# Kernel tuning notes

Hardware: AMD Instinct MI355X
Metric: run time of the kernel (lower is better)

The kernel has to match this reference:

```python
import jax, jax.numpy as jnp
import numpy as np

B, C, H, W = 4, 384, 56, 56
K, S = 5, 7


def setup_inputs() -> dict:
    key = jax.random.key(0)
    k1, k2, k3, k4, k5 = jax.random.split(key, 5)
    x = jax.random.normal(k1, (B, C, H, W), dtype=jnp.float32)
    ctx = jax.random.normal(k2, (B, C, H, W), dtype=jnp.float32)
    # 1x1 conv weights stored as (out_ch, in_ch) matrices
    Wq = jax.random.normal(k3, (C // 2, C), dtype=jnp.float32) * (1.0 / np.sqrt(C))
    Wk = jax.random.normal(k4, (C // 2, C), dtype=jnp.float32) * (1.0 / np.sqrt(C))
    Wwd = jax.random.normal(k5, (K * K, S * S), dtype=jnp.float32) * (1.0 / np.sqrt(S * S))
    return {"x": x, "ctx": ctx, "Wq": Wq, "Wk": Wk, "Wwd": Wwd}


def reference(x, ctx, Wq, Wk, Wwd):
    b, c, h, w = x.shape
    kk = K
    # q: 1x1 conv then flatten spatial -> (B, C/2, HW)
    q = jnp.einsum('dc,bchw->bdhw', Wq, x).reshape(b, c // 2, h * w)
    # adaptive avg pool to S x S (H,W multiples of S -> uniform 8x8 bins)
    ctx_p = ctx.reshape(b, c, S, h // S, S, w // S).mean(axis=(3, 5))  # (B,C,S,S)
    kf = jnp.einsum('dc,bcst->bdst', Wk, ctx_p).reshape(b, c // 2, S * S)
    # attention over region centers: (B, HW, S*S)
    A = jax.nn.softmax(jnp.einsum('bdn,bds->bns', q, kf), axis=-1)
    # dynamic per-pixel kernels via 1x1 conv S*S -> k*k: (B, k*k, H, W)
    dyn = jnp.einsum('js,bns->bjn', Wwd, A).reshape(b, kk * kk, h, w)
    # unfold x (im2col with padding k//2) -> (B, C, k*k, H, W)
    pad = kk // 2
    xp = jnp.pad(x, ((0, 0), (0, 0), (pad, pad), (pad, pad)))
    patches = jnp.stack(
        [xp[:, :, i:i + h, j:j + w] for i in range(kk) for j in range(kk)], axis=2
    )
    # per-pixel weighted reduction over the k*k taps
    out = jnp.einsum('bcjhw,bjhw->bchw', patches, dyn)
    return out
```

## Files before the change

kernel.cpp:

```cpp
#include <hip/hip_runtime.h>

#define BB 4
#define CCH 384
#define HH 56
#define WWD 56
#define HW 3136
#define S2 49
#define S2P 52
#define D2 192
#define K2 25
#define XSP 20

__global__ __launch_bounds__(256) void gt_k(const float* __restrict__ Wk,
                                            const float* __restrict__ Wq,
                                            float* __restrict__ GT) {
    __shared__ float As[D2 * 16];
    __shared__ float Bs[D2 * 16];
    int bi = blockIdx.x % 24, bj = blockIdx.x / 24;
    int t = threadIdx.x;
    int tj = t & 15, ti = t >> 4;
#pragma unroll
    for (int k = 0; k < 3; k++) {
        int idx = t + 256 * k;
        int d = idx >> 2, q = idx & 3;
        *(float4*)&As[idx * 4] = *(const float4*)&Wk[(size_t)d * CCH + bi * 16 + 4 * q];
        *(float4*)&Bs[idx * 4] = *(const float4*)&Wq[(size_t)d * CCH + bj * 16 + 4 * q];
    }
    __syncthreads();
    float acc = 0.f;
#pragma unroll 8
    for (int d = 0; d < D2; d++)
        acc += As[d * 16 + ti] * Bs[d * 16 + tj];
    GT[(size_t)(bi * 16 + ti) * CCH + bj * 16 + tj] = acc;
}

__global__ __launch_bounds__(384) void mv_k(const float* __restrict__ ctx,
                                            const float* __restrict__ GTt,
                                            float* __restrict__ M) {
    __shared__ float v[CCH];
    int b = blockIdx.x / S2, s = blockIdx.x % S2;
    int t = threadIdx.x;
    int sy = s / 7, sx = s % 7;
    {
        const float* p = ctx + ((size_t)(b * CCH + t)) * HW + sy * 8 * WWD + sx * 8;
        float sum = 0.f;
#pragma unroll
        for (int r = 0; r < 8; r++) {
            float4 a = *(const float4*)(p + r * WWD);
            float4 c = *(const float4*)(p + r * WWD + 4);
            sum += a.x + a.y + a.z + a.w + c.x + c.y + c.z + c.w;
        }
        v[t] = sum * (1.f / 64.f);
    }
    __syncthreads();
    const float4* g4 = (const float4*)(GTt + (size_t)t * CCH);
    const float4* v4 = (const float4*)v;
    float s0 = 0.f, s1 = 0.f, s2 = 0.f, s3 = 0.f;
#pragma unroll 16
    for (int i = 0; i < CCH / 4; i++) {
        float4 gv = g4[i];
        float4 vq = v4[i];
        s0 += gv.x * vq.x; s1 += gv.y * vq.y;
        s2 += gv.z * vq.z; s3 += gv.w * vq.w;
    }
    float acc = (s0 + s1) + (s2 + s3);
    M[((size_t)(b * CCH + t)) * S2P + s] = acc;
    if (s < 3) M[((size_t)(b * CCH + t)) * S2P + 49 + s] = 0.f;
}

__global__ __launch_bounds__(256) void attn_k(const float* __restrict__ x,
                                              const float* __restrict__ M,
                                              const float* __restrict__ Wwd,
                                              float* __restrict__ dyn) {
    __shared__ __align__(16) float smem[96 * XSP + 96 * S2P];
    __shared__ __align__(16) float sc[16 * S2P];
    __shared__ __align__(16) float wl[K2 * S2P];
    float* xs  = smem;
    float* Ms  = smem + 96 * XSP;
    float* red = smem;

    int b  = blockIdx.x / 196;
    int n0 = (blockIdx.x % 196) * 16;
    int t  = threadIdx.x;
    int pxg = t & 3, sg = (t >> 2) & 3, slice = t >> 4;

    float4 acc4[4][4];
#pragma unroll
    for (int k = 0; k < 4; k++)
#pragma unroll
        for (int j = 0; j < 4; j++) acc4[k][j] = make_float4(0.f, 0.f, 0.f, 0.f);

    const float* xb = x + (size_t)b * CCH * HW + n0;
    const float* Mb = M + (size_t)b * CCH * S2P;

#pragma unroll
    for (int k = 0; k < 5; k++) {
        int i = t + 256 * k;
        int j = i / S2P, ss = i - j * S2P;
        wl[i] = (ss < S2) ? Wwd[j * S2 + ss] : 0.f;
    }
    if (t < 20) {
        int i = t + 1280;
        int j = i / S2P, ss = i - j * S2P;
        wl[i] = (ss < S2) ? Wwd[j * S2 + ss] : 0.f;
    }

    int r0 = t >> 2, cq = t & 3;
    int r1 = (t + 256) >> 2;
    float4 px0, px1, pm0, pm1, pm2, pm3, pm4;

#define ATTN_LOAD(c0)                                                          \
    {                                                                          \
        px0 = *(const float4*)&xb[(size_t)((c0) + r0) * HW + 4 * cq];          \
        if (t < 128)                                                           \
            px1 = *(const float4*)&xb[(size_t)((c0) + r1) * HW + 4 * cq];      \
        const float* srcm = Mb + (size_t)(c0) * S2P;                           \
        pm0 = *(const float4*)&srcm[4 * t];                                    \
        pm1 = *(const float4*)&srcm[4 * (t + 256)];                            \
        pm2 = *(const float4*)&srcm[4 * (t + 512)];                            \
        pm3 = *(const float4*)&srcm[4 * (t + 768)];                            \
        if (t < 224) pm4 = *(const float4*)&srcm[4 * (t + 1024)];              \
    }

#define ATTN_WRITE()                                                           \
    {                                                                          \
        *(float4*)&xs[r0 * XSP + 4 * cq] = px0;                                \
        if (t < 128) *(float4*)&xs[r1 * XSP + 4 * cq] = px1;                   \
        *(float4*)&Ms[4 * t] = pm0;                                            \
        *(float4*)&Ms[4 * (t + 256)] = pm1;                                    \
        *(float4*)&Ms[4 * (t + 512)] = pm2;                                    \
        *(float4*)&Ms[4 * (t + 768)] = pm3;                                    \
        if (t < 224) *(float4*)&Ms[4 * (t + 1024)] = pm4;                      \
    }

    ATTN_LOAD(0);
    for (int ch = 0; ch < 4; ch++) {
        ATTN_WRITE();
        __syncthreads();
        if (ch < 3) { ATTN_LOAD((ch + 1) * 96); }
        int rbase = 6 * slice;
#pragma unroll
        for (int m = 0; m < 6; m++) {
            int r = rbase + m;
            const float4 xv = *(const float4*)&xs[r * XSP + 4 * pxg];
#pragma unroll
            for (int k = 0; k < 3; k++) {
                int g = sg + 4 * k;
                const float4 mv = *(const float4*)&Ms[r * S2P + 4 * g];
                acc4[k][0].x += mv.x * xv.x; acc4[k][0].y += mv.x * xv.y;
                acc4[k][0].z += mv.x * xv.z; acc4[k][0].w += mv.x * xv.w;
                acc4[k][1].x += mv.y * xv.x; acc4[k][1].y += mv.y * xv.y;
                acc4[k][1].z += mv.y * xv.z; acc4[k][1].w += mv.y * xv.w;
                acc4[k][2].x += mv.z * xv.x; acc4[k][2].y += mv.z * xv.y;
                acc4[k][2].z += mv.z * xv.z; acc4[k][2].w += mv.z * xv.w;
                acc4[k][3].x += mv.w * xv.x; acc4[k][3].y += mv.w * xv.y;
                acc4[k][3].z += mv.w * xv.z; acc4[k][3].w += mv.w * xv.w;
            }
            if (sg == 0) {
                const float4 mv = *(const float4*)&Ms[r * S2P + 48];
                acc4[3][0].x += mv.x * xv.x; acc4[3][0].y += mv.x * xv.y;
                acc4[3][0].z += mv.x * xv.z; acc4[3][0].w += mv.x * xv.w;
                acc4[3][1].x += mv.y * xv.x; acc4[3][1].y += mv.y * xv.y;
                acc4[3][1].z += mv.y * xv.z; acc4[3][1].w += mv.y * xv.w;
                acc4[3][2].x += mv.z * xv.x; acc4[3][2].y += mv.z * xv.y;
                acc4[3][2].z += mv.z * xv.z; acc4[3][2].w += mv.z * xv.w;
                acc4[3][3].x += mv.w * xv.x; acc4[3][3].y += mv.w * xv.y;
                acc4[3][3].z += mv.w * xv.z; acc4[3][3].w += mv.w * xv.w;
            }
        }
        __syncthreads();
    }

#pragma unroll
    for (int k = 0; k < 4; k++)
#pragma unroll
        for (int j = 0; j < 4; j++) {
            acc4[k][j].x += __shfl_xor(acc4[k][j].x, 16);
            acc4[k][j].y += __shfl_xor(acc4[k][j].y, 16);
            acc4[k][j].z += __shfl_xor(acc4[k][j].z, 16);
            acc4[k][j].w += __shfl_xor(acc4[k][j].w, 16);
            acc4[k][j].x += __shfl_xor(acc4[k][j].x, 32);
            acc4[k][j].y += __shfl_xor(acc4[k][j].y, 32);
            acc4[k][j].z += __shfl_xor(acc4[k][j].z, 32);
            acc4[k][j].w += __shfl_xor(acc4[k][j].w, 32);
        }

    if ((t & 63) < 16) {
        int wv = t >> 6;
        float* rb = red + (size_t)wv * 16 * S2P;
#pragma unroll
        for (int k = 0; k < 4; k++) {
            int g = sg + 4 * k;
            if (g < 13) {
                *(float4*)&rb[(4 * pxg + 0) * S2P + 4 * g] =
                    make_float4(acc4[k][0].x, acc4[k][1].x, acc4[k][2].x, acc4[k][3].x);
                *(float4*)&rb[(4 * pxg + 1) * S2P + 4 * g] =
                    make_float4(acc4[k][0].y, acc4[k][1].y, acc4[k][2].y, acc4[k][3].y);
                *(float4*)&rb[(4 * pxg + 2) * S2P + 4 * g] =
                    make_float4(acc4[k][0].z, acc4[k][1].z, acc4[k][2].z, acc4[k][3].z);
                *(float4*)&rb[(4 * pxg + 3) * S2P + 4 * g] =
                    make_float4(acc4[k][0].w, acc4[k][1].w, acc4[k][2].w, acc4[k][3].w);
            }
        }
    }
    __syncthreads();

    if (t < 208) {
        int px = t / 13, q = t - px * 13;
        float4 ssum = make_float4(0.f, 0.f, 0.f, 0.f);
#pragma unroll
        for (int wv = 0; wv < 4; wv++) {
            float4 vv = *(float4*)&red[(size_t)(wv * 16 + px) * S2P + 4 * q];
            ssum.x += vv.x; ssum.y += vv.y; ssum.z += vv.z; ssum.w += vv.w;
        }
        *(float4*)&sc[px * S2P + 4 * q] = ssum;
    }
    __syncthreads();

    if (t < 128) {
        int px = t >> 3, li = t & 7;
        float mx = -3.4e38f;
#pragma unroll
        for (int k = 0; k < 7; k++) { int s = li + 8 * k; if (s < S2) mx = fmaxf(mx, sc[px * S2P + s]); }
        mx = fmaxf(mx, __shfl_xor(mx, 1, 8));
        mx = fmaxf(mx, __shfl_xor(mx, 2, 8));
        mx = fmaxf(mx, __shfl_xor(mx, 4, 8));
        float e[7]; float sum = 0.f;
#pragma unroll
        for (int k = 0; k < 7; k++) {
            int s = li + 8 * k;
            if (s < S2) { e[k] = __expf(sc[px * S2P + s] - mx); sum += e[k]; }
        }
        sum += __shfl_xor(sum, 1, 8);
        sum += __shfl_xor(sum, 2, 8);
        sum += __shfl_xor(sum, 4, 8);
        float inv = 1.f / sum;
#pragma unroll
        for (int k = 0; k < 7; k++) {
            int s = li + 8 * k;
            if (s < S2) sc[px * S2P + s] = e[k] * inv;
        }
    }
    __syncthreads();

    float* dynb = dyn + (size_t)b * K2 * HW + n0;
#pragma unroll
    for (int pass = 0; pass < 2; pass++) {
        int o = t + 256 * pass;
        if (pass == 0 || t < 144) {
            int j = o >> 4, px = o & 15;
            float a = 0.f;
#pragma unroll
            for (int q = 0; q < 13; q++) {
                float4 wv = *(float4*)&wl[j * S2P + 4 * q];
                float4 pv = *(float4*)&sc[px * S2P + 4 * q];
                a += wv.x * pv.x + wv.y * pv.y + wv.z * pv.z + wv.w * pv.w;
            }
            dynb[(size_t)j * HW + px] = a;
        }
    }
#undef ATTN_LOAD
#undef ATTN_WRITE
}

__global__ __launch_bounds__(256, 3) void out_k(const float* __restrict__ x,
                                                const float* __restrict__ dyn,
                                                float* __restrict__ out) {
    __shared__ float xt[16][12][60];
    int blk    = blockIdx.x;
    int stripe = blk % 7;
    int cg     = (blk / 7) % 24;
    int b      = blk / (7 * 24);
    int h0 = stripe * 8;
    int c0 = cg * 16;
    int t  = threadIdx.x;
    const float* xb = x + ((size_t)(b * CCH + c0)) * HW;

    if (t < 192) {
        int cc = t / 12, r = t % 12;
        xt[cc][r][0] = 0.f; xt[cc][r][1] = 0.f;
        xt[cc][r][58] = 0.f; xt[cc][r][59] = 0.f;
    }
#pragma unroll
    for (int k = 0; k < 11; k++) {
        int idx = t + 256 * k;
        if (k < 10 || t < 128) {
            int cc  = idx / 168;
            int rem = idx - cc * 168;
            int r   = rem / 14;
            int q   = rem - r * 14;
            int h   = h0 - 2 + r;
            float4 v = make_float4(0.f, 0.f, 0.f, 0.f);
            if ((unsigned)h < (unsigned)HH)
                v = *(const float4*)&xb[(size_t)cc * HW + h * WWD + 4 * q];
            xt[cc][r][2 + 4 * q + 0] = v.x;
            xt[cc][r][2 + 4 * q + 1] = v.y;
            xt[cc][r][2 + 4 * q + 2] = v.z;
            xt[cc][r][2 + 4 * q + 3] = v.w;
        }
    }

    bool act = t < 224;
    int w = t % 56;
    int u = t / 56;
    int n = (h0 + 2 * u) * WWD + w;
    float dv0[K2], dv1[K2];
    if (act) {
        const float* db = dyn + (size_t)b * K2 * HW + n;
#pragma unroll
        for (int j = 0; j < K2; j++) {
            dv0[j] = db[(size_t)j * HW];
            dv1[j] = db[(size_t)j * HW + WWD];
        }
    }
    __syncthreads();
    if (!act) return;

    float* ob = out + ((size_t)(b * CCH + c0)) * HW + n;
#pragma unroll
    for (int cc = 0; cc < 16; cc++) {
        float a0 = 0.f, a1 = 0.f;
#pragma unroll
        for (int rr = 0; rr < 6; rr++) {
            int lr = 2 * u + rr;
            float v0 = xt[cc][lr][w + 0];
            float v1 = xt[cc][lr][w + 1];
            float v2 = xt[cc][lr][w + 2];
            float v3 = xt[cc][lr][w + 3];
            float v4 = xt[cc][lr][w + 4];
            if (rr < 5) {
                int o5 = rr * 5;
                a0 += v0 * dv0[o5] + v1 * dv0[o5 + 1] + v2 * dv0[o5 + 2]
                    + v3 * dv0[o5 + 3] + v4 * dv0[o5 + 4];
            }
            if (rr >= 1) {
                int o5 = (rr - 1) * 5;
                a1 += v0 * dv1[o5] + v1 * dv1[o5 + 1] + v2 * dv1[o5 + 2]
                    + v3 * dv1[o5 + 3] + v4 * dv1[o5 + 4];
            }
        }
        ob[(size_t)cc * HW] = a0;
        ob[(size_t)cc * HW + WWD] = a1;
    }
}

extern "C" void kernel_launch(void* const* d_in, const int* in_sizes, int n_in,
                              void* d_out, int out_size, void* d_ws, size_t ws_size,
                              hipStream_t stream) {
    const float* x   = (const float*)d_in[0];
    const float* ctx = (const float*)d_in[1];
    const float* Wq  = (const float*)d_in[2];
    const float* Wk  = (const float*)d_in[3];
    const float* Wwd = (const float*)d_in[4];
    float* out = (float*)d_out;
    float* ws  = (float*)d_ws;

    float* GT  = ws;
    float* M   = ws + 147456;
    float* dyn = ws + 147456 + 79872;

    gt_k<<<24 * 24, 256, 0, stream>>>(Wq, Wk, GT);
    mv_k<<<BB * S2, 384, 0, stream>>>(ctx, GT, M);
    attn_k<<<BB * 196, 256, 0, stream>>>(x, M, Wwd, dyn);
    out_k<<<BB * 24 * 7, 256, 0, stream>>>(x, dyn, out);
}
```

Before: 158.6 us.

## Split pooling from GT matvec so each GT row is reused across pooled vectors

The fused pool-plus-matvec kernel is split into a pooling kernel that writes pooled context vectors to a workspace buffer, and a new matvec kernel where each thread computes one GT row against two pooled vectors. Before, every one of the 196 blocks re-read the whole GT matrix. Now each GT row is read by one block and combined with all batch-region vectors, which cuts redundant global and L2 traffic. The cost is an extra kernel launch and a round trip of the pooled buffer, which reuses the dyn workspace region.

```diff
diff --git a/kernel.cpp b/kernel.cpp
--- a/kernel.cpp
+++ b/kernel.cpp
@@ -34,38 +34,56 @@
     GT[(size_t)(bi * 16 + ti) * CCH + bj * 16 + tj] = acc;
 }
 
-__global__ __launch_bounds__(384) void mv_k(const float* __restrict__ ctx,
-                                            const float* __restrict__ GTt,
-                                            float* __restrict__ M) {
-    __shared__ float v[CCH];
-    int b = blockIdx.x / S2, s = blockIdx.x % S2;
+__global__ __launch_bounds__(384) void pool_k(const float* __restrict__ ctx,
+                                              float* __restrict__ P) {
+    int bs = blockIdx.x;
+    int b = bs / S2, s = bs - b * S2;
     int t = threadIdx.x;
     int sy = s / 7, sx = s % 7;
-    {
-        const float* p = ctx + ((size_t)(b * CCH + t)) * HW + sy * 8 * WWD + sx * 8;
-        float sum = 0.f;
-#pragma unroll
-        for (int r = 0; r < 8; r++) {
-            float4 a = *(const float4*)(p + r * WWD);
-            float4 c = *(const float4*)(p + r * WWD + 4);
-            sum += a.x + a.y + a.z + a.w + c.x + c.y + c.z + c.w;
-        }
-        v[t] = sum * (1.f / 64.f);
-    }
-    __syncthreads();
-    const float4* g4 = (const float4*)(GTt + (size_t)t * CCH);
-    const float4* v4 = (const float4*)v;
-    float s0 = 0.f, s1 = 0.f, s2 = 0.f, s3 = 0.f;
-#pragma unroll 16
+    const float* p = ctx + ((size_t)(b * CCH + t)) * HW + sy * 8 * WWD + sx * 8;
+    float sum = 0.f;
+#pragma unroll
+    for (int r = 0; r < 8; r++) {
+        float4 a  = *(const float4*)(p + r * WWD);
+        float4 c4 = *(const float4*)(p + r * WWD + 4);
+        sum += a.x + a.y + a.z + a.w + c4.x + c4.y + c4.z + c4.w;
+    }
+    P[(size_t)bs * CCH + t] = sum * (1.f / 64.f);
+}
+
+__global__ __launch_bounds__(256) void mv2_k(const float* __restrict__ GTt,
+                                             const float* __restrict__ P,
+                                             float* __restrict__ M) {
+    int t = threadIdx.x;
+    int r = blockIdx.x * 2 + (t >> 7);
+    int c = t & 127;
+    int bs0 = c, bs1 = c + 128;
+    bool has1 = (bs1 < BB * S2);
+    const float4* g4 = (const float4*)(GTt + (size_t)r * CCH);
+    const float4* p0 = (const float4*)(P + (size_t)bs0 * CCH);
+    const float4* p1 = (const float4*)(P + (size_t)(has1 ? bs1 : bs0) * CCH);
+    float a0 = 0.f, a1 = 0.f, a2 = 0.f, a3 = 0.f;
+#pragma unroll 8
     for (int i = 0; i < CCH / 4; i++) {
-        float4 gv = g4[i];
-        float4 vq = v4[i];
-        s0 += gv.x * vq.x; s1 += gv.y * vq.y;
-        s2 += gv.z * vq.z; s3 += gv.w * vq.w;
-    }
-    float acc = (s0 + s1) + (s2 + s3);
-    M[((size_t)(b * CCH + t)) * S2P + s] = acc;
-    if (s < 3) M[((size_t)(b * CCH + t)) * S2P + 49 + s] = 0.f;
+        float4 g  = g4[i];
+        float4 q0 = p0[i];
+        float4 q1 = p1[i];
+        a0 += g.x * q0.x + g.y * q0.y;
+        a1 += g.z * q0.z + g.w * q0.w;
+        a2 += g.x * q1.x + g.y * q1.y;
+        a3 += g.z * q1.z + g.w * q1.w;
+    }
+    int b0 = bs0 / S2, s0 = bs0 - b0 * S2;
+    M[((size_t)(b0 * CCH + r)) * S2P + s0] = a0 + a1;
+    if (has1) {
+        int b1 = bs1 / S2, s1 = bs1 - b1 * S2;
+        M[((size_t)(b1 * CCH + r)) * S2P + s1] = a2 + a3;
+    }
+    if (c >= 68 && c < 80) {
+        int rem = c - 68;
+        int bb = rem / 3, sp = 49 + rem % 3;
+        M[((size_t)(bb * CCH + r)) * S2P + sp] = 0.f;
+    }
 }
 
 __global__ __launch_bounds__(256) void attn_k(const float* __restrict__ x,
@@ -358,9 +376,11 @@
     float* GT  = ws;
     float* M   = ws + 147456;
     float* dyn = ws + 147456 + 79872;
+    float* P   = dyn;
 
     gt_k<<<24 * 24, 256, 0, stream>>>(Wq, Wk, GT);
-    mv_k<<<BB * S2, 384, 0, stream>>>(ctx, GT, M);
+    pool_k<<<BB * S2, 384, 0, stream>>>(ctx, P);
+    mv2_k<<<CCH / 2, 256, 0, stream>>>(GT, P, M);
     attn_k<<<BB * 196, 256, 0, stream>>>(x, M, Wwd, dyn);
     out_k<<<BB * 24 * 7, 256, 0, stream>>>(x, dyn, out);
 }
```

After: 168.5 us. 6.2% more time.
